# Optimization experiments

Hardware: AMD Instinct MI355X
Metric: run time of the kernel (lower is better)

The kernel has to match this reference:

```python
import jax, jax.numpy as jnp
import numpy as np

V, D, H, L, B, S = 8192, 128, 8, 2, 1, 128
HD = D // H
HID = int(8 * D / 3)
EPS = 1e-6


def setup_inputs() -> dict:
    key = jax.random.key(0)
    ks = jax.random.split(key, 12)
    sc = 0.02
    return {
        "idx": jax.random.randint(ks[0], (B, S), 0, V),
        "w_raw": jax.random.normal(ks[1], (D, V), jnp.float32) * sc,
        "norm1_w": jnp.ones((L, D), jnp.float32),
        "norm2_w": jnp.ones((L, D), jnp.float32),
        "wq": jax.random.normal(ks[2], (L, D, D), jnp.float32) * sc,
        "wk": jax.random.normal(ks[3], (L, D, D), jnp.float32) * sc,
        "wv": jax.random.normal(ks[4], (L, D, D), jnp.float32) * sc,
        "wo": jax.random.normal(ks[5], (L, D, D), jnp.float32) * sc,
        "w1": jax.random.normal(ks[6], (L, D, HID), jnp.float32) * sc,
        "w3": jax.random.normal(ks[7], (L, D, HID), jnp.float32) * sc,
        "w2": jax.random.normal(ks[8], (L, HID, D), jnp.float32) * sc,
        "final_norm_w": jnp.ones((D,), jnp.float32),
    }


def rmsnorm(x, w):
    return x * jax.lax.rsqrt(jnp.mean(x * x, axis=-1, keepdims=True) + EPS) * w


def rope_cos_sin(seqlen, hd):
    inv = 1.0 / (10000.0 ** (jnp.arange(0, hd, 2, dtype=jnp.float32) / hd))
    t = jnp.arange(seqlen, dtype=jnp.float32)
    f = jnp.outer(t, inv)  # (S, hd/2)
    return jnp.cos(f), jnp.sin(f)


def apply_rope(x, cos, sin):
    # x: (B,S,H,HD); interleaved complex pairs as in Llama
    x0, x1 = x[..., 0::2], x[..., 1::2]
    c = cos[None, :, None, :]
    s = sin[None, :, None, :]
    r0 = x0 * c - x1 * s
    r1 = x0 * s + x1 * c
    return jnp.stack([r0, r1], axis=-1).reshape(x.shape)


def forward(idx, w_raw, norm1_w, norm2_w, wq, wk, wv, wo, w1, w2, w3, final_norm_w):
    Wemb = jax.nn.sigmoid(w_raw)                 # (D,V)
    x = Wemb.T[idx]                              # Yoneda one-hot @ W.T == gather -> (B,S,D)
    cos, sin = rope_cos_sin(S, HD)
    causal = jnp.tril(jnp.ones((S, S), bool))[None, None]  # (1,1,S,S)
    scale = 1.0 / jnp.sqrt(jnp.float32(HD))
    for i in range(L):
        # Multi-Universe attention (heads == universes), RoPE, causal SDPA
        h = rmsnorm(x, norm1_w[i])
        q = (h @ wq[i]).reshape(B, S, H, HD)
        k = (h @ wk[i]).reshape(B, S, H, HD)
        v = (h @ wv[i]).reshape(B, S, H, HD)
        q = apply_rope(q, cos, sin)
        k = apply_rope(k, cos, sin)
        scores = jnp.einsum("bihd,bjhd->bhij", q, k) * scale
        scores = jnp.where(causal, scores, jnp.float32(-1e9))
        attn = jax.nn.softmax(scores, axis=-1)
        o = jnp.einsum("bhij,bjhd->bihd", attn, v).reshape(B, S, D) @ wo[i]
        x = x + o
        # SwiGLU FFN
        h2 = rmsnorm(x, norm2_w[i])
        x = x + (jax.nn.silu(h2 @ w1[i]) * (h2 @ w3[i])) @ w2[i]
    x_norm = rmsnorm(x, final_norm_w)
    # Godel-Heyting reachability head
    x_n = x_norm / jnp.linalg.norm(x_norm, axis=-1, keepdims=True)      # (B,S,D)
    v_n = (Wemb / jnp.linalg.norm(Wemb, axis=0, keepdims=True)).T        # (V,D)
    a = x_n[:, :, None, :]                                               # (B,S,1,D)
    b = v_n[None, None, :, :]                                            # (1,1,V,D)
    # strict Godel implication: a => b = 1 if a <= b else b
    imp = jnp.where(a <= b, jnp.float32(1.0), b)                         # (B,S,V,D)
    logits = jnp.clip(imp.mean(axis=-1), 1e-6, 1.0 - 1e-6)               # (B,S,V)
    return logits


def reference(idx, w_raw, norm1_w, norm2_w, wq, wk, wv, wo, w1, w2, w3, final_norm_w):
    return forward(idx, w_raw, norm1_w, norm2_w, wq, wk, wv, wo, w1, w2, w3, final_norm_w)
```

## Files before the change

kernel.cpp:

```cpp
#include <hip/hip_runtime.h>
#include <math.h>

#define V 8192
#define D 128
#define NH 8
#define HD 16
#define SEQ 128
#define HID 341
#define EPS 1e-6f

__device__ __forceinline__ float sigm(float x) { return 1.0f / (1.0f + expf(-x)); }

__device__ __forceinline__ float block_sum256(float v, float* scratch) {
    #pragma unroll
    for (int m = 32; m > 0; m >>= 1) v += __shfl_xor(v, m);
    if ((threadIdx.x & 63) == 0) scratch[threadIdx.x >> 6] = v;
    __syncthreads();
    float s = (scratch[0] + scratch[1]) + (scratch[2] + scratch[3]);
    __syncthreads();
    return s;
}

__device__ __forceinline__ void qkv_rope(const float* hr, const float* wq,
                                         const float* wk, const float* wv, int s,
                                         float* qrow, float* krow,
                                         float (*vpart)[D], float* qo, float* ko,
                                         float* vo) {
    int t = threadIdx.x;
    int col = t & 127, half = t >> 7;
    {
        const float* w = (t < 128) ? wq : wk;
        float a0 = 0, a1 = 0;
        #pragma unroll 8
        for (int d = 0; d < D; d += 2) {
            a0 += hr[d] * w[d * D + col];
            a1 += hr[d + 1] * w[(d + 1) * D + col];
        }
        if (t < 128) qrow[col] = a0 + a1;
        else krow[col] = a0 + a1;
    }
    {
        int dlo = half * 64;
        float a0 = 0, a1 = 0;
        #pragma unroll 8
        for (int d = dlo; d < dlo + 64; d += 2) {
            a0 += hr[d] * wv[d * D + col];
            a1 += hr[d + 1] * wv[(d + 1) * D + col];
        }
        vpart[half][col] = a0 + a1;
    }
    __syncthreads();
    if (t < 128) {
        vo[s * D + t] = vpart[0][t] + vpart[1][t];
        int c = t & (HD - 1);
        int m = c >> 1;
        float fr = (float)s * expf(-(float)m * 1.15129254649702283e+00f);
        float cs = cosf(fr), sn = sinf(fr);
        int base = t & ~1;
        float qe = qrow[base], qod = qrow[base + 1];
        float ke = krow[base], kod = krow[base + 1];
        qo[s * D + t] = (c & 1) ? (qe * sn + qod * cs) : (qe * cs - qod * sn);
        ko[s * D + t] = (c & 1) ? (ke * sn + kod * cs) : (ke * cs - kod * sn);
    }
}

__global__ __launch_bounds__(256) void k_embed_qkv(
    const int* __restrict__ idx, const float* __restrict__ w_raw,
    const float* __restrict__ wq, const float* __restrict__ wk,
    const float* __restrict__ wv, const float* __restrict__ n1w,
    float* __restrict__ x, float* __restrict__ q, float* __restrict__ k,
    float* __restrict__ v) {
    __shared__ float hr[D], qrow[D], krow[D], vpart[2][D], scr[4];
    int s = blockIdx.x, t = threadIdx.x;
    float xv = 0.f;
    if (t < 128) {
        xv = sigm(w_raw[t * V + idx[s]]);
        x[s * D + t] = xv;
    }
    float ss = block_sum256(xv * xv, scr);
    float r = 1.0f / sqrtf(ss * (1.0f / D) + EPS);
    if (t < 128) hr[t] = xv * r * n1w[t];
    __syncthreads();
    qkv_rope(hr, wq, wk, wv, s, qrow, krow, vpart, q, k, v);
}

template <int MODE>
__global__ __launch_bounds__(256) void k_layer(
    const float* __restrict__ q, const float* __restrict__ kg,
    const float* __restrict__ vg, float* __restrict__ x,
    const float* __restrict__ wo, const float* __restrict__ n2w,
    const float* __restrict__ w1, const float* __restrict__ w3,
    const float* __restrict__ w2, const float* __restrict__ wq,
    const float* __restrict__ wk, const float* __restrict__ wv,
    const float* __restrict__ n1w, float* __restrict__ qo, float* __restrict__ ko,
    float* __restrict__ vo, const float* __restrict__ fw, float* __restrict__ xng) {
    __shared__ float ps[NH][SEQ + 1];
    __shared__ float qs[D], orow[D], h2[D];
    __shared__ float part[2][D];
    __shared__ float qrow[D], krow[D];
    __shared__ float afA[HID], afB[HID], af[HID];
    __shared__ float rl[NH];
    __shared__ float scr[4];
    int s = blockIdx.x, t = threadIdx.x;
    int col = t & 127, half = t >> 7;

    float xr = 0.f;
    if (t < 128) {
        qs[t] = q[s * D + t];
        xr = x[s * D + t];
    }
    __syncthreads();

    {
        int j = col;
        #pragma unroll
        for (int u = 0; u < 4; ++u) {
            int h = half + 2 * u;
            const float4* kp = (const float4*)&kg[j * D + h * HD];
            float4 ka = kp[0], kb = kp[1], kc = kp[2], kd = kp[3];
            const float* qh = &qs[h * HD];
            float acc = ka.x * qh[0] + ka.y * qh[1] + ka.z * qh[2] + ka.w * qh[3] +
                        kb.x * qh[4] + kb.y * qh[5] + kb.z * qh[6] + kb.w * qh[7] +
                        kc.x * qh[8] + kc.y * qh[9] + kc.z * qh[10] + kc.w * qh[11] +
                        kd.x * qh[12] + kd.y * qh[13] + kd.z * qh[14] + kd.w * qh[15];
            ps[h][j] = acc * 0.25f;
        }
    }
    __syncthreads();

    {
        int h = t >> 5, lane = t & 31;
        float pm = -1e30f;
        for (int j = lane; j <= s; j += 32) pm = fmaxf(pm, ps[h][j]);
        #pragma unroll
        for (int m = 16; m > 0; m >>= 1) pm = fmaxf(pm, __shfl_xor(pm, m, 32));
        float psum = 0.f;
        for (int j = lane; j <= s; j += 32) {
            float e = expf(ps[h][j] - pm);
            ps[h][j] = e;
            psum += e;
        }
        #pragma unroll
        for (int m = 16; m > 0; m >>= 1) psum += __shfl_xor(psum, m, 32);
        if (lane == 0) rl[h] = 1.0f / psum;
    }
    __syncthreads();

    {
        int h = col >> 4;
        int jlo = half * 64;
        int jhi = (s < jlo + 63) ? s : (jlo + 63);
        float a0 = 0, a1 = 0, a2 = 0, a3 = 0;
        int j = jlo;
        #pragma unroll 4
        for (; j + 3 <= jhi; j += 4) {
            a0 += ps[h][j] * vg[j * D + col];
            a1 += ps[h][j + 1] * vg[(j + 1) * D + col];
            a2 += ps[h][j + 2] * vg[(j + 2) * D + col];
            a3 += ps[h][j + 3] * vg[(j + 3) * D + col];
        }
        for (; j <= jhi; ++j) a0 += ps[h][j] * vg[j * D + col];
        part[half][col] = (a0 + a1) + (a2 + a3);
    }
    __syncthreads();
    if (t < 128) orow[t] = (part[0][t] + part[1][t]) * rl[t >> 4];
    __syncthreads();

    {
        int dlo = half * 64;
        float a0 = 0, a1 = 0;
        #pragma unroll 8
        for (int d = dlo; d < dlo + 64; d += 2) {
            a0 += orow[d] * wo[d * D + col];
            a1 += orow[d + 1] * wo[(d + 1) * D + col];
        }
        part[half][col] = a0 + a1;
    }
    __syncthreads();
    float xn = 0.f;
    if (t < 128) xn = xr + part[0][t] + part[1][t];
    float ss2 = block_sum256((t < 128) ? xn * xn : 0.f, scr);
    float r2 = 1.0f / sqrtf(ss2 * (1.0f / D) + EPS);
    if (t < 128) h2[t] = xn * r2 * n2w[t];
    __syncthreads();

    for (int task = t; task < 2 * HID; task += 256) {
        int mat = task >= HID;
        int c2 = mat ? (task - HID) : task;
        const float* w = mat ? w3 : w1;
        float a0 = 0, a1 = 0;
        #pragma unroll 8
        for (int d = 0; d < D; d += 2) {
            a0 += h2[d] * w[d * HID + c2];
            a1 += h2[d + 1] * w[(d + 1) * HID + c2];
        }
        if (mat) afB[c2] = a0 + a1;
        else afA[c2] = a0 + a1;
    }
    __syncthreads();
    for (int c2 = t; c2 < HID; c2 += 256) {
        float a1v = afA[c2];
        af[c2] = (a1v / (1.0f + expf(-a1v))) * afB[c2];
    }
    __syncthreads();

    {
        int lo = half * 171;
        int hi = half ? HID : 171;
        float a0 = 0, a1 = 0;
        int tt = lo;
        #pragma unroll 8
        for (; tt + 1 < hi; tt += 2) {
            a0 += af[tt] * w2[tt * D + col];
            a1 += af[tt + 1] * w2[(tt + 1) * D + col];
        }
        for (; tt < hi; ++tt) a0 += af[tt] * w2[tt * D + col];
        part[half][col] = a0 + a1;
    }
    __syncthreads();
    float x2 = 0.f;
    if (t < 128) {
        x2 = xn + part[0][t] + part[1][t];
        if (MODE == 0) x[s * D + t] = x2;
    }

    if constexpr (MODE == 0) {
        float ss = block_sum256((t < 128) ? x2 * x2 : 0.f, scr);
        float r = 1.0f / sqrtf(ss * (1.0f / D) + EPS);
        if (t < 128) h2[t] = x2 * r * n1w[t];
        __syncthreads();
        qkv_rope(h2, wq, wk, wv, s, qrow, krow, part, qo, ko, vo);
    } else {
        float ss = block_sum256((t < 128) ? x2 * x2 : 0.f, scr);
        float r = 1.0f / sqrtf(ss * (1.0f / D) + EPS);
        float y = (t < 128) ? x2 * r * fw[t] : 0.f;
        float nn = block_sum256(y * y, scr);
        if (t < 128) xng[t * SEQ + s] = y / sqrtf(nn);
    }
}

__global__ __launch_bounds__(256) void k_logits(const float* __restrict__ xng,
                                                const float* __restrict__ w_raw,
                                                float* __restrict__ out) {
    __shared__ float xs[D * 64];
    __shared__ float vs[D * 32];
    __shared__ float nred[256];
    __shared__ float invn_s[32];
    int t = threadIdx.x;
    int sbase = (blockIdx.x & 1) * 64;
    int vbase = (blockIdx.x >> 1) * 32;
    for (int i = t; i < D * 64; i += 256) {
        int d = i >> 6, s2 = i & 63;
        xs[i] = xng[d * SEQ + sbase + s2];
    }
    for (int i = t; i < D * 32; i += 256) {
        int d = i >> 5, jj = i & 31;
        vs[i] = sigm(w_raw[d * V + vbase + jj]);
    }
    __syncthreads();
    {
        int colc = t & 31, dp = t >> 5;
        float p = 0.f;
        for (int u = 0; u < 16; ++u) {
            float vv = vs[(dp * 16 + u) * 32 + colc];
            p += vv * vv;
        }
        nred[t] = p;
    }
    __syncthreads();
    if (t < 32) {
        float sum = 0.f;
        for (int u = 0; u < 8; ++u) sum += nred[u * 32 + t];
        invn_s[t] = 1.0f / sqrtf(sum);
    }
    __syncthreads();
    for (int i = t; i < D * 32; i += 256) vs[i] *= invn_s[i & 31];
    __syncthreads();
    int vg = t & 15;
    int sg = t >> 4;
    float acc[4][2] = {};
    for (int d = 0; d < D; ++d) {
        float4 xq = *(const float4*)&xs[d * 64 + sg * 4];
        float2 vq = *(const float2*)&vs[d * 32 + vg * 2];
        acc[0][0] += (xq.x <= vq.x) ? 1.0f : vq.x;
        acc[0][1] += (xq.x <= vq.y) ? 1.0f : vq.y;
        acc[1][0] += (xq.y <= vq.x) ? 1.0f : vq.x;
        acc[1][1] += (xq.y <= vq.y) ? 1.0f : vq.y;
        acc[2][0] += (xq.z <= vq.x) ? 1.0f : vq.x;
        acc[2][1] += (xq.z <= vq.y) ? 1.0f : vq.y;
        acc[3][0] += (xq.w <= vq.x) ? 1.0f : vq.x;
        acc[3][1] += (xq.w <= vq.y) ? 1.0f : vq.y;
    }
    const float inv128 = 1.0f / 128.0f;
    #pragma unroll
    for (int si = 0; si < 4; ++si) {
        int s = sbase + sg * 4 + si;
        float2 ov;
        ov.x = fminf(fmaxf(acc[si][0] * inv128, 1e-6f), 1.0f - 1e-6f);
        ov.y = fminf(fmaxf(acc[si][1] * inv128, 1e-6f), 1.0f - 1e-6f);
        *(float2*)&out[s * V + vbase + vg * 2] = ov;
    }
}

extern "C" void kernel_launch(void* const* d_in, const int* in_sizes, int n_in,
                              void* d_out, int out_size, void* d_ws, size_t ws_size,
                              hipStream_t stream) {
    const int* idx = (const int*)d_in[0];
    const float* w_raw = (const float*)d_in[1];
    const float* n1w = (const float*)d_in[2];
    const float* n2w = (const float*)d_in[3];
    const float* wq = (const float*)d_in[4];
    const float* wk = (const float*)d_in[5];
    const float* wv = (const float*)d_in[6];
    const float* wo = (const float*)d_in[7];
    const float* w1 = (const float*)d_in[8];
    const float* w3 = (const float*)d_in[9];
    const float* w2 = (const float*)d_in[10];
    const float* fnw = (const float*)d_in[11];
    float* out = (float*)d_out;
    float* ws = (float*)d_ws;

    float* x   = ws;
    float* q1  = ws + 16384;
    float* k1  = ws + 32768;
    float* v1  = ws + 49152;
    float* q2  = ws + 65536;
    float* k2  = ws + 81920;
    float* v2  = ws + 98304;
    float* xng = ws + 114688;

    k_embed_qkv<<<dim3(SEQ), dim3(256), 0, stream>>>(idx, w_raw, wq, wk, wv, n1w,
                                                     x, q1, k1, v1);
    k_layer<0><<<dim3(SEQ), dim3(256), 0, stream>>>(
        q1, k1, v1, x, wo, n2w, w1, w3, w2,
        wq + D * D, wk + D * D, wv + D * D, n1w + D, q2, k2, v2,
        (const float*)nullptr, (float*)nullptr);
    k_layer<1><<<dim3(SEQ), dim3(256), 0, stream>>>(
        q2, k2, v2, x, wo + D * D, n2w + D, w1 + D * HID, w3 + D * HID,
        w2 + HID * D, (const float*)nullptr, (const float*)nullptr,
        (const float*)nullptr, (const float*)nullptr, (float*)nullptr,
        (float*)nullptr, (float*)nullptr, fnw, xng);
    k_logits<<<dim3(512), dim3(256), 0, stream>>>(xng, w_raw, out);
}
```

Before: 159.2 us.

## Warm caches with extra prefetch blocks and preload weights into registers

Extra blocks are added to the embedding/QKV launch. They stream all of w_raw and the layer weights through the cache hierarchy, so later kernels (including the logits head) hit in cache. Inside the layer kernels, K, V, Wo and Wq/Wk/Wv columns are loaded into registers up front to overlap global latency with the reduction and sync. The PV loop now runs a fixed 64 iterations over zero-masked scores, and expf is replaced with __expf. Accumulator unrolling is widened throughout. The trade-off is heavy register pressure from large per-thread arrays, extra bandwidth spent on warming reads, and the fixed PV loop does wasted work for early rows.

```diff
diff --git a/kernel.cpp b/kernel.cpp
--- a/kernel.cpp
+++ b/kernel.cpp
@@ -9,7 +9,7 @@
 #define HID 341
 #define EPS 1e-6f
 
-__device__ __forceinline__ float sigm(float x) { return 1.0f / (1.0f + expf(-x)); }
+__device__ __forceinline__ float sigm(float x) { return 1.0f / (1.0f + __expf(-x)); }
 
 __device__ __forceinline__ float block_sum256(float v, float* scratch) {
     #pragma unroll
@@ -21,37 +21,80 @@
     return s;
 }
 
-__device__ __forceinline__ void qkv_rope(const float* hr, const float* wq,
-                                         const float* wk, const float* wv, int s,
-                                         float* qrow, float* krow,
-                                         float (*vpart)[D], float* qo, float* ko,
-                                         float* vo) {
+__global__ __launch_bounds__(256, 1) void k_embed_qkv(
+    const int* __restrict__ idx, const float* __restrict__ w_raw,
+    const float* __restrict__ wq, const float* __restrict__ wk,
+    const float* __restrict__ wv, const float* __restrict__ n1w,
+    const float* __restrict__ w1, const float* __restrict__ w3,
+    const float* __restrict__ w2, const float* __restrict__ wo,
+    float* __restrict__ x, float* __restrict__ q, float* __restrict__ k,
+    float* __restrict__ v, float* __restrict__ sink) {
     int t = threadIdx.x;
-    int col = t & 127, half = t >> 7;
-    {
-        const float* w = (t < 128) ? wq : wk;
-        float a0 = 0, a1 = 0;
-        #pragma unroll 8
-        for (int d = 0; d < D; d += 2) {
-            a0 += hr[d] * w[d * D + col];
-            a1 += hr[d + 1] * w[(d + 1) * D + col];
-        }
-        if (t < 128) qrow[col] = a0 + a1;
-        else krow[col] = a0 + a1;
-    }
-    {
-        int dlo = half * 64;
-        float a0 = 0, a1 = 0;
-        #pragma unroll 8
-        for (int d = dlo; d < dlo + 64; d += 2) {
-            a0 += hr[d] * wv[d * D + col];
-            a1 += hr[d + 1] * wv[(d + 1) * D + col];
-        }
-        vpart[half][col] = a0 + a1;
-    }
+    if (blockIdx.x >= SEQ) {
+        int g = (blockIdx.x - SEQ) * 256 + t;
+        float acc = 0.f;
+        const float4* p = (const float4*)w_raw;
+        for (int i = g; i < 262144; i += 65536) {
+            float4 u = p[i];
+            acc += u.x + u.y + u.z + u.w;
+        }
+        p = (const float4*)w1;
+        if (g < 21824) { float4 u = p[g]; acc += u.x + u.y + u.z + u.w; }
+        p = (const float4*)w3;
+        if (g < 21824) { float4 u = p[g]; acc += u.x + u.y + u.z + u.w; }
+        p = (const float4*)w2;
+        if (g < 21824) { float4 u = p[g]; acc += u.x + u.y + u.z + u.w; }
+        p = (const float4*)wq;
+        if (g < 8192) { float4 u = p[g]; acc += u.x + u.y + u.z + u.w; }
+        p = (const float4*)wk;
+        if (g < 8192) { float4 u = p[g]; acc += u.x + u.y + u.z + u.w; }
+        p = (const float4*)wv;
+        if (g < 8192) { float4 u = p[g]; acc += u.x + u.y + u.z + u.w; }
+        p = (const float4*)wo;
+        if (g < 8192) { float4 u = p[g]; acc += u.x + u.y + u.z + u.w; }
+        if (acc == 1234.5678f) sink[0] = acc;
+        return;
+    }
+    __shared__ float hr[D], qrow[D], krow[D], vpart[2][D], scr[4];
+    int s = blockIdx.x;
+    int col = t & 127, half = t >> 7, dlo = half * 64;
+    float xv = 0.f;
+    if (t < 128) xv = sigm(w_raw[t * V + idx[s]]);
+    float wpre[128];
+    const float* wsel = (t < 128) ? wq : wk;
+    #pragma unroll
+    for (int d = 0; d < 128; ++d) wpre[d] = wsel[d * D + col];
+    float wvpre[64];
+    #pragma unroll
+    for (int d = 0; d < 64; ++d) wvpre[d] = wv[(dlo + d) * D + col];
+    if (t < 128) x[s * D + t] = xv;
+    float ss = block_sum256(xv * xv, scr);
+    float r = 1.0f / sqrtf(ss * (1.0f / D) + EPS);
+    if (t < 128) hr[t] = xv * r * n1w[t];
+    __syncthreads();
+    float a0 = 0, a1 = 0, a2 = 0, a3 = 0;
+    #pragma unroll
+    for (int d = 0; d < 128; d += 4) {
+        a0 += hr[d] * wpre[d];
+        a1 += hr[d + 1] * wpre[d + 1];
+        a2 += hr[d + 2] * wpre[d + 2];
+        a3 += hr[d + 3] * wpre[d + 3];
+    }
+    float qk = (a0 + a1) + (a2 + a3);
+    float b0 = 0, b1 = 0, b2 = 0, b3 = 0;
+    #pragma unroll
+    for (int d = 0; d < 64; d += 4) {
+        b0 += hr[dlo + d] * wvpre[d];
+        b1 += hr[dlo + d + 1] * wvpre[d + 1];
+        b2 += hr[dlo + d + 2] * wvpre[d + 2];
+        b3 += hr[dlo + d + 3] * wvpre[d + 3];
+    }
+    vpart[half][col] = (b0 + b1) + (b2 + b3);
+    if (t < 128) qrow[col] = qk;
+    else krow[col] = qk;
     __syncthreads();
     if (t < 128) {
-        vo[s * D + t] = vpart[0][t] + vpart[1][t];
+        v[s * D + t] = vpart[0][t] + vpart[1][t];
         int c = t & (HD - 1);
         int m = c >> 1;
         float fr = (float)s * expf(-(float)m * 1.15129254649702283e+00f);
@@ -59,33 +102,13 @@
         int base = t & ~1;
         float qe = qrow[base], qod = qrow[base + 1];
         float ke = krow[base], kod = krow[base + 1];
-        qo[s * D + t] = (c & 1) ? (qe * sn + qod * cs) : (qe * cs - qod * sn);
-        ko[s * D + t] = (c & 1) ? (ke * sn + kod * cs) : (ke * cs - kod * sn);
+        q[s * D + t] = (c & 1) ? (qe * sn + qod * cs) : (qe * cs - qod * sn);
+        k[s * D + t] = (c & 1) ? (ke * sn + kod * cs) : (ke * cs - kod * sn);
     }
 }
 
-__global__ __launch_bounds__(256) void k_embed_qkv(
-    const int* __restrict__ idx, const float* __restrict__ w_raw,
-    const float* __restrict__ wq, const float* __restrict__ wk,
-    const float* __restrict__ wv, const float* __restrict__ n1w,
-    float* __restrict__ x, float* __restrict__ q, float* __restrict__ k,
-    float* __restrict__ v) {
-    __shared__ float hr[D], qrow[D], krow[D], vpart[2][D], scr[4];
-    int s = blockIdx.x, t = threadIdx.x;
-    float xv = 0.f;
-    if (t < 128) {
-        xv = sigm(w_raw[t * V + idx[s]]);
-        x[s * D + t] = xv;
-    }
-    float ss = block_sum256(xv * xv, scr);
-    float r = 1.0f / sqrtf(ss * (1.0f / D) + EPS);
-    if (t < 128) hr[t] = xv * r * n1w[t];
-    __syncthreads();
-    qkv_rope(hr, wq, wk, wv, s, qrow, krow, vpart, q, k, v);
-}
-
 template <int MODE>
-__global__ __launch_bounds__(256) void k_layer(
+__global__ __launch_bounds__(256, 1) void k_layer(
     const float* __restrict__ q, const float* __restrict__ kg,
     const float* __restrict__ vg, float* __restrict__ x,
     const float* __restrict__ wo, const float* __restrict__ n2w,
@@ -97,34 +120,45 @@
     __shared__ float ps[NH][SEQ + 1];
     __shared__ float qs[D], orow[D], h2[D];
     __shared__ float part[2][D];
-    __shared__ float qrow[D], krow[D];
     __shared__ float afA[HID], afB[HID], af[HID];
     __shared__ float rl[NH];
     __shared__ float scr[4];
     int s = blockIdx.x, t = threadIdx.x;
     int col = t & 127, half = t >> 7;
-
-    float xr = 0.f;
+    int jlo = half * 64, dlo = half * 64;
+
+    float qv = 0.f, xr = 0.f;
     if (t < 128) {
-        qs[t] = q[s * D + t];
+        qv = q[s * D + t];
         xr = x[s * D + t];
     }
-    __syncthreads();
-
-    {
-        int j = col;
-        #pragma unroll
-        for (int u = 0; u < 4; ++u) {
-            int h = half + 2 * u;
-            const float4* kp = (const float4*)&kg[j * D + h * HD];
-            float4 ka = kp[0], kb = kp[1], kc = kp[2], kd = kp[3];
-            const float* qh = &qs[h * HD];
-            float acc = ka.x * qh[0] + ka.y * qh[1] + ka.z * qh[2] + ka.w * qh[3] +
-                        kb.x * qh[4] + kb.y * qh[5] + kb.z * qh[6] + kb.w * qh[7] +
-                        kc.x * qh[8] + kc.y * qh[9] + kc.z * qh[10] + kc.w * qh[11] +
-                        kd.x * qh[12] + kd.y * qh[13] + kd.z * qh[14] + kd.w * qh[15];
-            ps[h][j] = acc * 0.25f;
-        }
+    float4 kp[4][4];
+    #pragma unroll
+    for (int u = 0; u < 4; ++u) {
+        const float4* p = (const float4*)&kg[col * D + (half + 2 * u) * HD];
+        kp[u][0] = p[0]; kp[u][1] = p[1]; kp[u][2] = p[2]; kp[u][3] = p[3];
+    }
+    float vpre[64];
+    #pragma unroll
+    for (int j = 0; j < 64; ++j) vpre[j] = vg[(jlo + j) * D + col];
+    float wopre[64];
+    #pragma unroll
+    for (int u = 0; u < 64; ++u) wopre[u] = wo[(dlo + u) * D + col];
+
+    if (t < 128) qs[t] = qv;
+    __syncthreads();
+
+    #pragma unroll
+    for (int u = 0; u < 4; ++u) {
+        int h = half + 2 * u;
+        const float* qh = &qs[h * HD];
+        float acc = kp[u][0].x * qh[0] + kp[u][0].y * qh[1] + kp[u][0].z * qh[2] +
+                    kp[u][0].w * qh[3] + kp[u][1].x * qh[4] + kp[u][1].y * qh[5] +
+                    kp[u][1].z * qh[6] + kp[u][1].w * qh[7] + kp[u][2].x * qh[8] +
+                    kp[u][2].y * qh[9] + kp[u][2].z * qh[10] + kp[u][2].w * qh[11] +
+                    kp[u][3].x * qh[12] + kp[u][3].y * qh[13] + kp[u][3].z * qh[14] +
+                    kp[u][3].w * qh[15];
+        ps[h][col] = (col <= s) ? acc * 0.25f : 0.f;
     }
     __syncthreads();
 
@@ -136,7 +170,7 @@
         for (int m = 16; m > 0; m >>= 1) pm = fmaxf(pm, __shfl_xor(pm, m, 32));
         float psum = 0.f;
         for (int j = lane; j <= s; j += 32) {
-            float e = expf(ps[h][j] - pm);
+            float e = __expf(ps[h][j] - pm);
             ps[h][j] = e;
             psum += e;
         }
@@ -148,18 +182,14 @@
 
     {
         int h = col >> 4;
-        int jlo = half * 64;
-        int jhi = (s < jlo + 63) ? s : (jlo + 63);
         float a0 = 0, a1 = 0, a2 = 0, a3 = 0;
-        int j = jlo;
-        #pragma unroll 4
-        for (; j + 3 <= jhi; j += 4) {
-            a0 += ps[h][j] * vg[j * D + col];
-            a1 += ps[h][j + 1] * vg[(j + 1) * D + col];
-            a2 += ps[h][j + 2] * vg[(j + 2) * D + col];
-            a3 += ps[h][j + 3] * vg[(j + 3) * D + col];
-        }
-        for (; j <= jhi; ++j) a0 += ps[h][j] * vg[j * D + col];
+        #pragma unroll
+        for (int j = 0; j < 64; j += 4) {
+            a0 += ps[h][jlo + j] * vpre[j];
+            a1 += ps[h][jlo + j + 1] * vpre[j + 1];
+            a2 += ps[h][jlo + j + 2] * vpre[j + 2];
+            a3 += ps[h][jlo + j + 3] * vpre[j + 3];
+        }
         part[half][col] = (a0 + a1) + (a2 + a3);
     }
     __syncthreads();
@@ -167,12 +197,11 @@
     __syncthreads();
 
     {
-        int dlo = half * 64;
         float a0 = 0, a1 = 0;
-        #pragma unroll 8
-        for (int d = dlo; d < dlo + 64; d += 2) {
-            a0 += orow[d] * wo[d * D + col];
-            a1 += orow[d + 1] * wo[(d + 1) * D + col];
+        #pragma unroll
+        for (int u = 0; u < 64; u += 2) {
+            a0 += orow[dlo + u] * wopre[u];
+            a1 += orow[dlo + u + 1] * wopre[u + 1];
         }
         part[half][col] = a0 + a1;
     }
@@ -188,34 +217,38 @@
         int mat = task >= HID;
         int c2 = mat ? (task - HID) : task;
         const float* w = mat ? w3 : w1;
-        float a0 = 0, a1 = 0;
+        float a0 = 0, a1 = 0, a2 = 0, a3 = 0;
         #pragma unroll 8
-        for (int d = 0; d < D; d += 2) {
+        for (int d = 0; d < D; d += 4) {
             a0 += h2[d] * w[d * HID + c2];
             a1 += h2[d + 1] * w[(d + 1) * HID + c2];
-        }
-        if (mat) afB[c2] = a0 + a1;
-        else afA[c2] = a0 + a1;
+            a2 += h2[d + 2] * w[(d + 2) * HID + c2];
+            a3 += h2[d + 3] * w[(d + 3) * HID + c2];
+        }
+        if (mat) afB[c2] = (a0 + a1) + (a2 + a3);
+        else afA[c2] = (a0 + a1) + (a2 + a3);
     }
     __syncthreads();
     for (int c2 = t; c2 < HID; c2 += 256) {
         float a1v = afA[c2];
-        af[c2] = (a1v / (1.0f + expf(-a1v))) * afB[c2];
+        af[c2] = (a1v / (1.0f + __expf(-a1v))) * afB[c2];
     }
     __syncthreads();
 
     {
-        int lo = half * 171;
-        int hi = half ? HID : 171;
-        float a0 = 0, a1 = 0;
+        int lo = half ? 171 : 0;
+        int hi = half ? 341 : 171;
+        float a0 = 0, a1 = 0, a2 = 0, a3 = 0;
         int tt = lo;
         #pragma unroll 8
-        for (; tt + 1 < hi; tt += 2) {
+        for (; tt + 3 < hi; tt += 4) {
             a0 += af[tt] * w2[tt * D + col];
             a1 += af[tt + 1] * w2[(tt + 1) * D + col];
+            a2 += af[tt + 2] * w2[(tt + 2) * D + col];
+            a3 += af[tt + 3] * w2[(tt + 3) * D + col];
         }
         for (; tt < hi; ++tt) a0 += af[tt] * w2[tt * D + col];
-        part[half][col] = a0 + a1;
+        part[half][col] = (a0 + a1) + (a2 + a3);
     }
     __syncthreads();
     float x2 = 0.f;
@@ -224,15 +257,47 @@
         if (MODE == 0) x[s * D + t] = x2;
     }
 
+    float ss = block_sum256((t < 128) ? x2 * x2 : 0.f, scr);
+    float r = 1.0f / sqrtf(ss * (1.0f / D) + EPS);
+
     if constexpr (MODE == 0) {
-        float ss = block_sum256((t < 128) ? x2 * x2 : 0.f, scr);
-        float r = 1.0f / sqrtf(ss * (1.0f / D) + EPS);
         if (t < 128) h2[t] = x2 * r * n1w[t];
         __syncthreads();
-        qkv_rope(h2, wq, wk, wv, s, qrow, krow, part, qo, ko, vo);
+        const float* wsel = (t < 128) ? wq : wk;
+        float a0 = 0, a1 = 0, a2 = 0, a3 = 0;
+        #pragma unroll 8
+        for (int d = 0; d < D; d += 4) {
+            a0 += h2[d] * wsel[d * D + col];
+            a1 += h2[d + 1] * wsel[(d + 1) * D + col];
+            a2 += h2[d + 2] * wsel[(d + 2) * D + col];
+            a3 += h2[d + 3] * wsel[(d + 3) * D + col];
+        }
+        float qk = (a0 + a1) + (a2 + a3);
+        float b0 = 0, b1 = 0, b2 = 0, b3 = 0;
+        #pragma unroll 8
+        for (int d = dlo; d < dlo + 64; d += 4) {
+            b0 += h2[d] * wv[d * D + col];
+            b1 += h2[d + 1] * wv[(d + 1) * D + col];
+            b2 += h2[d + 2] * wv[(d + 2) * D + col];
+            b3 += h2[d + 3] * wv[(d + 3) * D + col];
+        }
+        part[half][col] = (b0 + b1) + (b2 + b3);
+        if (t < 128) qs[col] = qk;
+        else orow[col] = qk;
+        __syncthreads();
+        if (t < 128) {
+            vo[s * D + t] = part[0][t] + part[1][t];
+            int c = t & (HD - 1);
+            int mm = c >> 1;
+            float fr = (float)s * expf(-(float)mm * 1.15129254649702283e+00f);
+            float cs = cosf(fr), sn = sinf(fr);
+            int base = t & ~1;
+            float qe = qs[base], qod = qs[base + 1];
+            float ke = orow[base], kod = orow[base + 1];
+            qo[s * D + t] = (c & 1) ? (qe * sn + qod * cs) : (qe * cs - qod * sn);
+            ko[s * D + t] = (c & 1) ? (ke * sn + kod * cs) : (ke * cs - kod * sn);
+        }
     } else {
-        float ss = block_sum256((t < 128) ? x2 * x2 : 0.f, scr);
-        float r = 1.0f / sqrtf(ss * (1.0f / D) + EPS);
         float y = (t < 128) ? x2 * r * fw[t] : 0.f;
         float nn = block_sum256(y * y, scr);
         if (t < 128) xng[t * SEQ + s] = y / sqrtf(nn);
@@ -320,17 +385,18 @@
     float* out = (float*)d_out;
     float* ws = (float*)d_ws;
 
-    float* x   = ws;
-    float* q1  = ws + 16384;
-    float* k1  = ws + 32768;
-    float* v1  = ws + 49152;
-    float* q2  = ws + 65536;
-    float* k2  = ws + 81920;
-    float* v2  = ws + 98304;
-    float* xng = ws + 114688;
-
-    k_embed_qkv<<<dim3(SEQ), dim3(256), 0, stream>>>(idx, w_raw, wq, wk, wv, n1w,
-                                                     x, q1, k1, v1);
+    float* x    = ws;
+    float* q1   = ws + 16384;
+    float* k1   = ws + 32768;
+    float* v1   = ws + 49152;
+    float* q2   = ws + 65536;
+    float* k2   = ws + 81920;
+    float* v2   = ws + 98304;
+    float* xng  = ws + 114688;
+    float* sink = ws + 131072;
+
+    k_embed_qkv<<<dim3(SEQ + 256), dim3(256), 0, stream>>>(
+        idx, w_raw, wq, wk, wv, n1w, w1, w3, w2, wo, x, q1, k1, v1, sink);
     k_layer<0><<<dim3(SEQ), dim3(256), 0, stream>>>(
         q1, k1, v1, x, wo, n2w, w1, w3, w2,
         wq + D * D, wk + D * D, wv + D * D, n1w + D, q2, k2, v2,
```

After: 146.4 us. 8.0% less time.

## Fuse embed and both layers into one persistent kernel with grid barriers

Applied to the files above, without the earlier changes.

Replaces the three per-layer launches with a single 128-block, 512-thread kernel that synchronises layers through an atomic grid barrier in workspace. Q stays in shared memory instead of going through global memory, and the softmax is rewritten to use all 64 lanes with masking. K/V/Wo columns are prefetched into registers before the attention math. At the start, every block touches all of w_raw and the layer weights to warm L2 for the later logits stage. The aim is to remove launch gaps and global round-trips, at the cost of higher register pressure, a spin barrier that needs all blocks to be resident at once, and extra upfront reads.

```diff
diff --git a/kernel.cpp b/kernel.cpp
--- a/kernel.cpp
+++ b/kernel.cpp
@@ -8,235 +8,324 @@
 #define SEQ 128
 #define HID 341
 #define EPS 1e-6f
-
-__device__ __forceinline__ float sigm(float x) { return 1.0f / (1.0f + expf(-x)); }
-
-__device__ __forceinline__ float block_sum256(float v, float* scratch) {
+#define NBLK 128
+#define NTHR 512
+#define POISONU 0xAAAAAAAAu
+
+__device__ __forceinline__ float sigm(float x) { return 1.0f / (1.0f + __expf(-x)); }
+
+struct SM {
+    float ps[NH][SEQ + 2];
+    float parts4[4][D];
+    float pB[3][2][D];
+    float qs[D], qrow[D], krow[D], orow[D], h2[D], xrow[D];
+    float afA[HID], afB[HID], af[HID];
+    float rl[NH];
+    float scr[8];
+};
+
+__device__ __forceinline__ float block_sum512(float v, float* scr) {
     #pragma unroll
     for (int m = 32; m > 0; m >>= 1) v += __shfl_xor(v, m);
-    if ((threadIdx.x & 63) == 0) scratch[threadIdx.x >> 6] = v;
-    __syncthreads();
-    float s = (scratch[0] + scratch[1]) + (scratch[2] + scratch[3]);
+    if ((threadIdx.x & 63) == 0) scr[threadIdx.x >> 6] = v;
+    __syncthreads();
+    float s = ((scr[0] + scr[1]) + (scr[2] + scr[3])) + ((scr[4] + scr[5]) + (scr[6] + scr[7]));
     __syncthreads();
     return s;
 }
 
-__device__ __forceinline__ void qkv_rope(const float* hr, const float* wq,
-                                         const float* wk, const float* wv, int s,
-                                         float* qrow, float* krow,
-                                         float (*vpart)[D], float* qo, float* ko,
-                                         float* vo) {
-    int t = threadIdx.x;
-    int col = t & 127, half = t >> 7;
-    {
-        const float* w = (t < 128) ? wq : wk;
+__device__ __forceinline__ void grid_barrier(unsigned* bar, unsigned target) {
+    __threadfence();
+    __syncthreads();
+    if (threadIdx.x == 0) {
+        unsigned old = atomicAdd(&bar[0], 1u);
+        if (old == (unsigned)(NBLK - 1)) {
+            atomicExch(&bar[0], 0u);
+            __threadfence();
+            atomicAdd(&bar[1], 1u);
+        }
+        while (__hip_atomic_load(&bar[1], __ATOMIC_ACQUIRE, __HIP_MEMORY_SCOPE_AGENT) < target) {
+            __builtin_amdgcn_s_sleep(2);
+        }
+    }
+    __syncthreads();
+    __threadfence();
+}
+
+__device__ __forceinline__ void qkv_rope_512(int s, int t, SM& S,
+                                             const float* __restrict__ wq,
+                                             const float* __restrict__ wk,
+                                             const float* __restrict__ wv,
+                                             float* __restrict__ koutg,
+                                             float* __restrict__ voutg) {
+    int col = t & 127;
+    const float* h = S.h2;
+    if (t < 256) {
+        const float* Wa = (t < 128) ? wq : wk;
+        const float* Wb = (t < 128) ? wk : wv;
+        float a0 = 0, a1 = 0, b0 = 0, b1 = 0;
+        #pragma unroll 8
+        for (int u = 0; u < 64; u += 2) {
+            a0 += h[u] * Wa[u * D + col];
+            a1 += h[u + 1] * Wa[(u + 1) * D + col];
+            b0 += h[64 + u] * Wb[(64 + u) * D + col];
+            b1 += h[64 + u + 1] * Wb[(64 + u + 1) * D + col];
+        }
+        S.pB[(t < 128) ? 0 : 1][0][col] = a0 + a1;
+        S.pB[(t < 128) ? 1 : 2][1][col] = b0 + b1;
+    } else {
+        const float* Wa = (t < 384) ? wv : wq;
+        int dlo = (t < 384) ? 0 : 64;
         float a0 = 0, a1 = 0;
         #pragma unroll 8
-        for (int d = 0; d < D; d += 2) {
-            a0 += hr[d] * w[d * D + col];
-            a1 += hr[d + 1] * w[(d + 1) * D + col];
-        }
-        if (t < 128) qrow[col] = a0 + a1;
-        else krow[col] = a0 + a1;
-    }
-    {
-        int dlo = half * 64;
-        float a0 = 0, a1 = 0;
-        #pragma unroll 8
-        for (int d = dlo; d < dlo + 64; d += 2) {
-            a0 += hr[d] * wv[d * D + col];
-            a1 += hr[d + 1] * wv[(d + 1) * D + col];
-        }
-        vpart[half][col] = a0 + a1;
+        for (int u = 0; u < 64; u += 2) {
+            a0 += h[dlo + u] * Wa[(dlo + u) * D + col];
+            a1 += h[dlo + u + 1] * Wa[(dlo + u + 1) * D + col];
+        }
+        S.pB[(t < 384) ? 2 : 0][(t < 384) ? 0 : 1][col] = a0 + a1;
     }
     __syncthreads();
     if (t < 128) {
-        vo[s * D + t] = vpart[0][t] + vpart[1][t];
+        float qv = S.pB[0][0][t] + S.pB[0][1][t];
+        float kv = S.pB[1][0][t] + S.pB[1][1][t];
+        float vv = S.pB[2][0][t] + S.pB[2][1][t];
+        voutg[s * D + t] = vv;
+        S.qrow[t] = qv;
+        S.krow[t] = kv;
+    }
+    __syncthreads();
+    if (t < 128) {
         int c = t & (HD - 1);
         int m = c >> 1;
         float fr = (float)s * expf(-(float)m * 1.15129254649702283e+00f);
         float cs = cosf(fr), sn = sinf(fr);
         int base = t & ~1;
-        float qe = qrow[base], qod = qrow[base + 1];
-        float ke = krow[base], kod = krow[base + 1];
-        qo[s * D + t] = (c & 1) ? (qe * sn + qod * cs) : (qe * cs - qod * sn);
-        ko[s * D + t] = (c & 1) ? (ke * sn + kod * cs) : (ke * cs - kod * sn);
-    }
-}
-
-__global__ __launch_bounds__(256) void k_embed_qkv(
-    const int* __restrict__ idx, const float* __restrict__ w_raw,
-    const float* __restrict__ wq, const float* __restrict__ wk,
-    const float* __restrict__ wv, const float* __restrict__ n1w,
-    float* __restrict__ x, float* __restrict__ q, float* __restrict__ k,
-    float* __restrict__ v) {
-    __shared__ float hr[D], qrow[D], krow[D], vpart[2][D], scr[4];
-    int s = blockIdx.x, t = threadIdx.x;
-    float xv = 0.f;
-    if (t < 128) {
-        xv = sigm(w_raw[t * V + idx[s]]);
-        x[s * D + t] = xv;
-    }
-    float ss = block_sum256(xv * xv, scr);
-    float r = 1.0f / sqrtf(ss * (1.0f / D) + EPS);
-    if (t < 128) hr[t] = xv * r * n1w[t];
-    __syncthreads();
-    qkv_rope(hr, wq, wk, wv, s, qrow, krow, vpart, q, k, v);
+        float qe = S.qrow[base], qod = S.qrow[base + 1];
+        float ke = S.krow[base], kod = S.krow[base + 1];
+        S.qs[t] = (c & 1) ? (qe * sn + qod * cs) : (qe * cs - qod * sn);
+        koutg[s * D + t] = (c & 1) ? (ke * sn + kod * cs) : (ke * cs - kod * sn);
+    }
 }
 
 template <int MODE>
-__global__ __launch_bounds__(256) void k_layer(
-    const float* __restrict__ q, const float* __restrict__ kg,
-    const float* __restrict__ vg, float* __restrict__ x,
+__device__ __forceinline__ void layer_phase(
+    int s, int t, SM& S, const float* __restrict__ kg, const float* __restrict__ vg,
     const float* __restrict__ wo, const float* __restrict__ n2w,
     const float* __restrict__ w1, const float* __restrict__ w3,
     const float* __restrict__ w2, const float* __restrict__ wq,
     const float* __restrict__ wk, const float* __restrict__ wv,
-    const float* __restrict__ n1w, float* __restrict__ qo, float* __restrict__ ko,
-    float* __restrict__ vo, const float* __restrict__ fw, float* __restrict__ xng) {
-    __shared__ float ps[NH][SEQ + 1];
-    __shared__ float qs[D], orow[D], h2[D];
-    __shared__ float part[2][D];
-    __shared__ float qrow[D], krow[D];
-    __shared__ float afA[HID], afB[HID], af[HID];
-    __shared__ float rl[NH];
-    __shared__ float scr[4];
-    int s = blockIdx.x, t = threadIdx.x;
-    int col = t & 127, half = t >> 7;
-
-    float xr = 0.f;
-    if (t < 128) {
-        qs[t] = q[s * D + t];
-        xr = x[s * D + t];
-    }
-    __syncthreads();
-
-    {
-        int j = col;
+    const float* __restrict__ n1w, float* __restrict__ kout, float* __restrict__ vout,
+    const float* __restrict__ fw, float* __restrict__ xng) {
+    int col = t & 127, grp = t >> 7;
+    float4 ka0, ka1, ka2, ka3, kb0, kb1, kb2, kb3;
+    {
+        const float4* p = (const float4*)&kg[col * D + grp * HD];
+        ka0 = p[0]; ka1 = p[1]; ka2 = p[2]; ka3 = p[3];
+        const float4* p2 = (const float4*)&kg[col * D + (grp + 4) * HD];
+        kb0 = p2[0]; kb1 = p2[1]; kb2 = p2[2]; kb3 = p2[3];
+    }
+    float vpre[32], wopre[32];
+    #pragma unroll
+    for (int u = 0; u < 32; ++u) vpre[u] = vg[(grp * 32 + u) * D + col];
+    #pragma unroll
+    for (int u = 0; u < 32; ++u) wopre[u] = wo[(grp * 32 + u) * D + col];
+
+    {
+        const float* qh = &S.qs[grp * HD];
+        float a = ka0.x * qh[0] + ka0.y * qh[1] + ka0.z * qh[2] + ka0.w * qh[3] +
+                  ka1.x * qh[4] + ka1.y * qh[5] + ka1.z * qh[6] + ka1.w * qh[7] +
+                  ka2.x * qh[8] + ka2.y * qh[9] + ka2.z * qh[10] + ka2.w * qh[11] +
+                  ka3.x * qh[12] + ka3.y * qh[13] + ka3.z * qh[14] + ka3.w * qh[15];
+        const float* qh2 = &S.qs[(grp + 4) * HD];
+        float b = kb0.x * qh2[0] + kb0.y * qh2[1] + kb0.z * qh2[2] + kb0.w * qh2[3] +
+                  kb1.x * qh2[4] + kb1.y * qh2[5] + kb1.z * qh2[6] + kb1.w * qh2[7] +
+                  kb2.x * qh2[8] + kb2.y * qh2[9] + kb2.z * qh2[10] + kb2.w * qh2[11] +
+                  kb3.x * qh2[12] + kb3.y * qh2[13] + kb3.z * qh2[14] + kb3.w * qh2[15];
+        S.ps[grp][col] = (col <= s) ? a * 0.25f : 0.f;
+        S.ps[grp + 4][col] = (col <= s) ? b * 0.25f : 0.f;
+    }
+    __syncthreads();
+    {
+        int h = t >> 6, lane = t & 63;
+        float v0 = (lane <= s) ? S.ps[h][lane] : -1e30f;
+        float v1 = (lane + 64 <= s) ? S.ps[h][lane + 64] : -1e30f;
+        float pm = fmaxf(v0, v1);
         #pragma unroll
-        for (int u = 0; u < 4; ++u) {
-            int h = half + 2 * u;
-            const float4* kp = (const float4*)&kg[j * D + h * HD];
-            float4 ka = kp[0], kb = kp[1], kc = kp[2], kd = kp[3];
-            const float* qh = &qs[h * HD];
-            float acc = ka.x * qh[0] + ka.y * qh[1] + ka.z * qh[2] + ka.w * qh[3] +
-                        kb.x * qh[4] + kb.y * qh[5] + kb.z * qh[6] + kb.w * qh[7] +
-                        kc.x * qh[8] + kc.y * qh[9] + kc.z * qh[10] + kc.w * qh[11] +
-                        kd.x * qh[12] + kd.y * qh[13] + kd.z * qh[14] + kd.w * qh[15];
-            ps[h][j] = acc * 0.25f;
-        }
-    }
-    __syncthreads();
-
-    {
-        int h = t >> 5, lane = t & 31;
-        float pm = -1e30f;
-        for (int j = lane; j <= s; j += 32) pm = fmaxf(pm, ps[h][j]);
+        for (int m = 32; m > 0; m >>= 1) pm = fmaxf(pm, __shfl_xor(pm, m));
+        float e0 = (lane <= s) ? __expf(v0 - pm) : 0.f;
+        float e1 = (lane + 64 <= s) ? __expf(v1 - pm) : 0.f;
+        S.ps[h][lane] = e0;
+        S.ps[h][lane + 64] = e1;
+        float sm = e0 + e1;
         #pragma unroll
-        for (int m = 16; m > 0; m >>= 1) pm = fmaxf(pm, __shfl_xor(pm, m, 32));
-        float psum = 0.f;
-        for (int j = lane; j <= s; j += 32) {
-            float e = expf(ps[h][j] - pm);
-            ps[h][j] = e;
-            psum += e;
-        }
+        for (int m = 32; m > 0; m >>= 1) sm += __shfl_xor(sm, m);
+        if (lane == 0) S.rl[h] = 1.0f / sm;
+    }
+    __syncthreads();
+    {
+        int h = col >> 4, jlo = grp * 32;
+        float a0 = 0, a1 = 0, a2 = 0, a3 = 0;
         #pragma unroll
-        for (int m = 16; m > 0; m >>= 1) psum += __shfl_xor(psum, m, 32);
-        if (lane == 0) rl[h] = 1.0f / psum;
-    }
-    __syncthreads();
-
-    {
-        int h = col >> 4;
-        int jlo = half * 64;
-        int jhi = (s < jlo + 63) ? s : (jlo + 63);
+        for (int u = 0; u < 32; u += 4) {
+            a0 += S.ps[h][jlo + u] * vpre[u];
+            a1 += S.ps[h][jlo + u + 1] * vpre[u + 1];
+            a2 += S.ps[h][jlo + u + 2] * vpre[u + 2];
+            a3 += S.ps[h][jlo + u + 3] * vpre[u + 3];
+        }
+        S.parts4[grp][col] = (a0 + a1) + (a2 + a3);
+    }
+    __syncthreads();
+    if (t < 128)
+        S.orow[t] = (S.parts4[0][t] + S.parts4[1][t] + S.parts4[2][t] + S.parts4[3][t]) * S.rl[t >> 4];
+    __syncthreads();
+    {
+        int dlo = grp * 32;
+        float a0 = 0, a1 = 0;
+        #pragma unroll
+        for (int u = 0; u < 32; u += 2) {
+            a0 += S.orow[dlo + u] * wopre[u];
+            a1 += S.orow[dlo + u + 1] * wopre[u + 1];
+        }
+        S.parts4[grp][col] = a0 + a1;
+    }
+    __syncthreads();
+    float xn = 0.f;
+    if (t < 128)
+        xn = S.xrow[t] + S.parts4[0][t] + S.parts4[1][t] + S.parts4[2][t] + S.parts4[3][t];
+    float ss2 = block_sum512((t < 128) ? xn * xn : 0.f, S.scr);
+    float r2 = 1.0f / sqrtf(ss2 * (1.0f / D) + EPS);
+    if (t < 128) S.h2[t] = xn * r2 * n2w[t];
+    __syncthreads();
+    if (t < 170) {
+        float a0 = 0, a1 = 0, b0 = 0, b1 = 0;
+        #pragma unroll 8
+        for (int d = 0; d < D; d += 2) {
+            a0 += S.h2[d] * w1[d * HID + t];
+            a1 += S.h2[d + 1] * w1[(d + 1) * HID + t];
+            b0 += S.h2[d] * w3[d * HID + t + 171];
+            b1 += S.h2[d + 1] * w3[(d + 1) * HID + t + 171];
+        }
+        S.afA[t] = a0 + a1;
+        S.afB[t + 171] = b0 + b1;
+    } else if (t < 341) {
         float a0 = 0, a1 = 0, a2 = 0, a3 = 0;
-        int j = jlo;
-        #pragma unroll 4
-        for (; j + 3 <= jhi; j += 4) {
-            a0 += ps[h][j] * vg[j * D + col];
-            a1 += ps[h][j + 1] * vg[(j + 1) * D + col];
-            a2 += ps[h][j + 2] * vg[(j + 2) * D + col];
-            a3 += ps[h][j + 3] * vg[(j + 3) * D + col];
-        }
-        for (; j <= jhi; ++j) a0 += ps[h][j] * vg[j * D + col];
-        part[half][col] = (a0 + a1) + (a2 + a3);
-    }
-    __syncthreads();
-    if (t < 128) orow[t] = (part[0][t] + part[1][t]) * rl[t >> 4];
-    __syncthreads();
-
-    {
-        int dlo = half * 64;
-        float a0 = 0, a1 = 0;
-        #pragma unroll 8
-        for (int d = dlo; d < dlo + 64; d += 2) {
-            a0 += orow[d] * wo[d * D + col];
-            a1 += orow[d + 1] * wo[(d + 1) * D + col];
-        }
-        part[half][col] = a0 + a1;
-    }
-    __syncthreads();
-    float xn = 0.f;
-    if (t < 128) xn = xr + part[0][t] + part[1][t];
-    float ss2 = block_sum256((t < 128) ? xn * xn : 0.f, scr);
-    float r2 = 1.0f / sqrtf(ss2 * (1.0f / D) + EPS);
-    if (t < 128) h2[t] = xn * r2 * n2w[t];
-    __syncthreads();
-
-    for (int task = t; task < 2 * HID; task += 256) {
-        int mat = task >= HID;
-        int c2 = mat ? (task - HID) : task;
-        const float* w = mat ? w3 : w1;
-        float a0 = 0, a1 = 0;
-        #pragma unroll 8
-        for (int d = 0; d < D; d += 2) {
-            a0 += h2[d] * w[d * HID + c2];
-            a1 += h2[d + 1] * w[(d + 1) * HID + c2];
-        }
-        if (mat) afB[c2] = a0 + a1;
-        else afA[c2] = a0 + a1;
-    }
-    __syncthreads();
-    for (int c2 = t; c2 < HID; c2 += 256) {
-        float a1v = afA[c2];
-        af[c2] = (a1v / (1.0f + expf(-a1v))) * afB[c2];
-    }
-    __syncthreads();
-
-    {
-        int lo = half * 171;
-        int hi = half ? HID : 171;
-        float a0 = 0, a1 = 0;
+        #pragma unroll 8
+        for (int d = 0; d < D; d += 4) {
+            a0 += S.h2[d] * w1[d * HID + t];
+            a1 += S.h2[d + 1] * w1[(d + 1) * HID + t];
+            a2 += S.h2[d + 2] * w1[(d + 2) * HID + t];
+            a3 += S.h2[d + 3] * w1[(d + 3) * HID + t];
+        }
+        S.afA[t] = (a0 + a1) + (a2 + a3);
+    } else {
+        int c2 = t - 341;
+        float a0 = 0, a1 = 0, a2 = 0, a3 = 0;
+        #pragma unroll 8
+        for (int d = 0; d < D; d += 4) {
+            a0 += S.h2[d] * w3[d * HID + c2];
+            a1 += S.h2[d + 1] * w3[(d + 1) * HID + c2];
+            a2 += S.h2[d + 2] * w3[(d + 2) * HID + c2];
+            a3 += S.h2[d + 3] * w3[(d + 3) * HID + c2];
+        }
+        S.afB[c2] = (a0 + a1) + (a2 + a3);
+    }
+    __syncthreads();
+    if (t < 341) {
+        float a1v = S.afA[t];
+        S.af[t] = (a1v / (1.0f + __expf(-a1v))) * S.afB[t];
+    }
+    __syncthreads();
+    {
+        int lo = grp * 86;
+        int hi = lo + 86;
+        if (hi > HID) hi = HID;
+        float a0 = 0, a1 = 0, a2 = 0, a3 = 0;
         int tt = lo;
         #pragma unroll 8
-        for (; tt + 1 < hi; tt += 2) {
-            a0 += af[tt] * w2[tt * D + col];
-            a1 += af[tt + 1] * w2[(tt + 1) * D + col];
-        }
-        for (; tt < hi; ++tt) a0 += af[tt] * w2[tt * D + col];
-        part[half][col] = a0 + a1;
+        for (; tt + 3 < hi; tt += 4) {
+            a0 += S.af[tt] * w2[tt * D + col];
+            a1 += S.af[tt + 1] * w2[(tt + 1) * D + col];
+            a2 += S.af[tt + 2] * w2[(tt + 2) * D + col];
+            a3 += S.af[tt + 3] * w2[(tt + 3) * D + col];
+        }
+        for (; tt < hi; ++tt) a0 += S.af[tt] * w2[tt * D + col];
+        S.parts4[grp][col] = (a0 + a1) + (a2 + a3);
     }
     __syncthreads();
     float x2 = 0.f;
     if (t < 128) {
-        x2 = xn + part[0][t] + part[1][t];
-        if (MODE == 0) x[s * D + t] = x2;
-    }
-
+        x2 = xn + S.parts4[0][t] + S.parts4[1][t] + S.parts4[2][t] + S.parts4[3][t];
+        S.xrow[t] = x2;
+    }
+    float ss3 = block_sum512((t < 128) ? x2 * x2 : 0.f, S.scr);
+    float r3 = 1.0f / sqrtf(ss3 * (1.0f / D) + EPS);
     if constexpr (MODE == 0) {
-        float ss = block_sum256((t < 128) ? x2 * x2 : 0.f, scr);
-        float r = 1.0f / sqrtf(ss * (1.0f / D) + EPS);
-        if (t < 128) h2[t] = x2 * r * n1w[t];
+        if (t < 128) S.h2[t] = x2 * r3 * n1w[t];
         __syncthreads();
-        qkv_rope(h2, wq, wk, wv, s, qrow, krow, part, qo, ko, vo);
+        qkv_rope_512(s, t, S, wq, wk, wv, kout, vout);
     } else {
-        float ss = block_sum256((t < 128) ? x2 * x2 : 0.f, scr);
-        float r = 1.0f / sqrtf(ss * (1.0f / D) + EPS);
-        float y = (t < 128) ? x2 * r * fw[t] : 0.f;
-        float nn = block_sum256(y * y, scr);
+        float y = (t < 128) ? x2 * r3 * fw[t] : 0.f;
+        float nn = block_sum512(y * y, S.scr);
         if (t < 128) xng[t * SEQ + s] = y / sqrtf(nn);
     }
+}
+
+__global__ __launch_bounds__(512, 2) void k_mega(
+    const int* __restrict__ idx, const float* __restrict__ w_raw,
+    const float* __restrict__ n1w, const float* __restrict__ n2w,
+    const float* __restrict__ wq, const float* __restrict__ wk,
+    const float* __restrict__ wv, const float* __restrict__ wo,
+    const float* __restrict__ w1, const float* __restrict__ w3,
+    const float* __restrict__ w2, const float* __restrict__ fnw,
+    float* __restrict__ k1, float* __restrict__ v1, float* __restrict__ k2,
+    float* __restrict__ v2, float* __restrict__ xng, unsigned* __restrict__ bar,
+    float* __restrict__ sink) {
+    __shared__ SM S;
+    int t = threadIdx.x, s = blockIdx.x;
+    unsigned gen0 = 0;
+    if (t == 0) {
+        atomicCAS(&bar[0], POISONU, 0u);
+        atomicCAS(&bar[1], POISONU, 0u);
+        gen0 = __hip_atomic_load(&bar[1], __ATOMIC_RELAXED, __HIP_MEMORY_SCOPE_AGENT);
+    }
+    float xv = 0.f;
+    if (t < 128) xv = sigm(w_raw[t * V + idx[s]]);
+    float wacc = 0.f;
+    int g = s * NTHR + t;
+    {
+        const float4* p = (const float4*)w_raw;
+        #pragma unroll
+        for (int i = 0; i < 4; ++i) {
+            float4 u = p[g + i * 65536];
+            wacc += u.x + u.y + u.z + u.w;
+        }
+        if (g < 21824) {
+            float4 u = ((const float4*)w1)[g]; wacc += u.x + u.y + u.z + u.w;
+            float4 u2 = ((const float4*)w3)[g]; wacc += u2.x + u2.y + u2.z + u2.w;
+            float4 u3 = ((const float4*)w2)[g]; wacc += u3.x + u3.y + u3.z + u3.w;
+        }
+        if (g < 8192) {
+            float4 u = ((const float4*)wq)[g]; wacc += u.x + u.y + u.z + u.w;
+            float4 u2 = ((const float4*)wk)[g]; wacc += u2.x + u2.y + u2.z + u2.w;
+            float4 u3 = ((const float4*)wv)[g]; wacc += u3.x + u3.y + u3.z + u3.w;
+            float4 u4 = ((const float4*)wo)[g]; wacc += u4.x + u4.y + u4.z + u4.w;
+        }
+    }
+    if (t < 128) S.xrow[t] = xv;
+    float ss = block_sum512((t < 128) ? xv * xv : 0.f, S.scr);
+    float r = 1.0f / sqrtf(ss * (1.0f / D) + EPS);
+    if (t < 128) S.h2[t] = xv * r * n1w[t];
+    __syncthreads();
+    qkv_rope_512(s, t, S, wq, wk, wv, k1, v1);
+    if (wacc == 1234.5678f) sink[0] = wacc;
+    grid_barrier(bar, gen0 + 1u);
+    layer_phase<0>(s, t, S, k1, v1, wo, n2w, w1, w3, w2, wq + D * D, wk + D * D,
+                   wv + D * D, n1w + D, k2, v2, (const float*)nullptr, (float*)nullptr);
+    grid_barrier(bar, gen0 + 2u);
+    layer_phase<1>(s, t, S, k2, v2, wo + D * D, n2w + D, w1 + D * HID, w3 + D * HID,
+                   w2 + HID * D, (const float*)nullptr, (const float*)nullptr,
+                   (const float*)nullptr, (const float*)nullptr, (float*)nullptr,
+                   (float*)nullptr, fnw, xng);
 }
 
 __global__ __launch_bounds__(256) void k_logits(const float* __restrict__ xng,
@@ -320,25 +409,16 @@
     float* out = (float*)d_out;
     float* ws = (float*)d_ws;
 
-    float* x   = ws;
-    float* q1  = ws + 16384;
-    float* k1  = ws + 32768;
-    float* v1  = ws + 49152;
-    float* q2  = ws + 65536;
-    float* k2  = ws + 81920;
-    float* v2  = ws + 98304;
-    float* xng = ws + 114688;
-
-    k_embed_qkv<<<dim3(SEQ), dim3(256), 0, stream>>>(idx, w_raw, wq, wk, wv, n1w,
-                                                     x, q1, k1, v1);
-    k_layer<0><<<dim3(SEQ), dim3(256), 0, stream>>>(
-        q1, k1, v1, x, wo, n2w, w1, w3, w2,
-        wq + D * D, wk + D * D, wv + D * D, n1w + D, q2, k2, v2,
-        (const float*)nullptr, (float*)nullptr);
-    k_layer<1><<<dim3(SEQ), dim3(256), 0, stream>>>(
-        q2, k2, v2, x, wo + D * D, n2w + D, w1 + D * HID, w3 + D * HID,
-        w2 + HID * D, (const float*)nullptr, (const float*)nullptr,
-        (const float*)nullptr, (const float*)nullptr, (float*)nullptr,
-        (float*)nullptr, (float*)nullptr, fnw, xng);
+    float* k1 = ws;
+    float* v1 = ws + 16384;
+    float* k2 = ws + 32768;
+    float* v2 = ws + 49152;
+    float* xng = ws + 65536;
+    unsigned* bar = (unsigned*)(ws + 81920);
+    float* sink = ws + 81928;
+
+    k_mega<<<dim3(NBLK), dim3(NTHR), 0, stream>>>(idx, w_raw, n1w, n2w, wq, wk, wv,
+                                                  wo, w1, w3, w2, fnw, k1, v1, k2,
+                                                  v2, xng, bar, sink);
     k_logits<<<dim3(512), dim3(256), 0, stream>>>(xng, w_raw, out);
 }
```

After: 231.7 us. 1.46x slower.
